# Kernel optimization log

Hardware: AMD Instinct MI355X
Metric: run time of the kernel (lower is better)

Reference implementation:

```python
import jax, jax.numpy as jnp
import numpy as np
from jax import lax

EPS = 1e-5

def conv3x3(x, w):
    # x: (B,C,H,W), w: (O,I,3,3), stride 1, padding 1
    return lax.conv_general_dilated(x, w, (1, 1), 'SAME',
                                    dimension_numbers=('NCHW', 'OIHW', 'NCHW'))

def bn_eval(x, p):
    # p: (4, C) rows = scale, bias, running_mean, running_var (eval-mode BatchNorm2d)
    s, b, m, v = p[0], p[1], p[2], p[3]
    inv = s / jnp.sqrt(v + EPS)
    return (x - m[:, None, None]) * inv[:, None, None] + b[:, None, None]

def sobel_eem(x, wx, wy, bnx, bny):
    gx = bn_eval(conv3x3(x, wx), bnx)
    gy = bn_eval(conv3x3(x, wy), bny)
    return jnp.sqrt(gx * gx + gy * gy)

def conv1x1(x, w, b):
    # w: (O, I)
    return jnp.einsum('oi,bihw->bohw', w, x) + b[:, None, None]

def attend(x_q, x_kv, qw, qb, kw, kb, vw, vb, gamma):
    B, C, H, W = x_q.shape
    N = H * W
    q = conv1x1(x_q, qw, qb).reshape(B, -1, N)      # (B, Cq, N)
    k = conv1x1(x_kv, kw, kb).reshape(B, -1, N)     # (B, Cq, N)
    v = conv1x1(x_kv, vw, vb).reshape(B, C, N)      # (B, C, N)
    energy = jnp.einsum('bcq,bck->bqk', q, k)       # unscaled QK^T, (B, N, N)
    attn = jax.nn.softmax(energy, axis=-1)
    out = jnp.einsum('bck,bqk->bcq', v, attn)       # V @ attn^T
    out = out.reshape(B, C, H, W)
    return gamma * out + x_q

def setup_inputs() -> dict:
    key = jax.random.key(0)
    ks = jax.random.split(key, 24)
    C, Cq, B, H, W = 256, 32, 1, 64, 64
    f32 = jnp.float32
    def bn_params(k):
        k1, k2 = jax.random.split(k)
        scale = 1.0 + 0.1 * jax.random.normal(k1, (C,), f32)
        bias = 0.1 * jax.random.normal(k2, (C,), f32)
        mean = jnp.zeros((C,), f32)
        var = jnp.ones((C,), f32)
        return jnp.stack([scale, bias, mean, var])
    return {
        'x1': jax.random.normal(ks[0], (B, C, H, W), f32),
        'x2': jax.random.normal(ks[1], (B, C, H, W), f32),
        'sx1_w': 0.05 * jax.random.normal(ks[2], (C, C, 3, 3), f32),
        'sy1_w': 0.05 * jax.random.normal(ks[3], (C, C, 3, 3), f32),
        'bn1x': bn_params(ks[4]), 'bn1y': bn_params(ks[5]),
        'sx2_w': 0.05 * jax.random.normal(ks[6], (C, C, 3, 3), f32),
        'sy2_w': 0.05 * jax.random.normal(ks[7], (C, C, 3, 3), f32),
        'bn2x': bn_params(ks[8]), 'bn2y': bn_params(ks[9]),
        'q1_w': 0.02 * jax.random.normal(ks[10], (Cq, C), f32),
        'q1_b': jnp.zeros((Cq,), f32),
        'k1_w': 0.02 * jax.random.normal(ks[11], (Cq, C), f32),
        'k1_b': jnp.zeros((Cq,), f32),
        'v1_w': 0.02 * jax.random.normal(ks[12], (C, C), f32),
        'v1_b': jnp.zeros((C,), f32),
        'q2_w': 0.02 * jax.random.normal(ks[13], (Cq, C), f32),
        'q2_b': jnp.zeros((Cq,), f32),
        'k2_w': 0.02 * jax.random.normal(ks[14], (Cq, C), f32),
        'k2_b': jnp.zeros((Cq,), f32),
        'v2_w': 0.02 * jax.random.normal(ks[15], (C, C), f32),
        'v2_b': jnp.zeros((C,), f32),
        'gamma1': jnp.ones((1,), f32),
        'gamma2': jnp.ones((1,), f32),
    }

def reference(x1, x2, sx1_w, sy1_w, bn1x, bn1y, sx2_w, sy2_w, bn2x, bn2y,
              q1_w, q1_b, k1_w, k1_b, v1_w, v1_b,
              q2_w, q2_b, k2_w, k2_b, v2_w, v2_b, gamma1, gamma2):
    xf1 = sobel_eem(x1, sx1_w, sy1_w, bn1x, bn1y)
    xf2 = sobel_eem(x2, sx2_w, sy2_w, bn2x, bn2y)
    # cross_value=True: K and V both come from the other modality's edge features
    out1 = attend(x1, xf2, q1_w, q1_b, k1_w, k1_b, v1_w, v1_b, gamma1)
    out2 = attend(x2, xf1, q2_w, q2_b, k2_w, k2_b, v2_w, v2_b, gamma2)
    return (out1, out2)
```

## Files before the change

### kernel.cpp

```cpp
#include <hip/hip_runtime.h>
#include <hip/hip_bf16.h>
#include <math.h>

#define CC 256
#define CQn 32
#define HH 64
#define WW 64
#define NN 4096
#define EPSF 1e-5f

typedef __hip_bfloat16 bf16;

typedef __attribute__((ext_vector_type(8))) short bf16x8v;
typedef __attribute__((ext_vector_type(4))) float f32x4v;

__device__ __forceinline__ float b2f(bf16 v) { return __bfloat162float(v); }
__device__ __forceinline__ bf16 f2b(float v) { return __float2bfloat16(v); }

template<typename T> __device__ __forceinline__ float ldf(const T* p, size_t i);
template<> __device__ __forceinline__ float ldf<float>(const float* p, size_t i) { return p[i]; }
template<> __device__ __forceinline__ float ldf<bf16>(const bf16* p, size_t i)  { return b2f(p[i]); }

__device__ __forceinline__ void stf(float* p, size_t i, float v) { p[i] = v; }
__device__ __forceinline__ void stf(bf16* p, size_t i, float v)  { p[i] = f2b(v); }

__global__ __launch_bounds__(256)
void detect_kernel(const unsigned short* __restrict__ x1, int* __restrict__ flag)
{
    __shared__ int bad;
    if (threadIdx.x == 0) bad = 0;
    __syncthreads();
    int mybad = 0;
    for (int i = threadIdx.x; i < 16384; i += 256) {
        unsigned short u = x1[i];
        if ((u & 0x7F80u) == 0x7F80u) mybad = 1;
    }
    if (mybad) atomicOr(&bad, 1);
    __syncthreads();
    if (threadIdx.x == 0) *flag = bad ? 1 : 0;
}

__global__ __launch_bounds__(256)
void transpose_kernel(const int* __restrict__ dflag,
                      const bf16* __restrict__ x, bf16* __restrict__ xT)
{
    if (*dflag != 0) return;
    const int ci0 = blockIdx.x * 64;
    const int p0  = blockIdx.y * 64;
    const int t = threadIdx.x;
    const int r0 = t >> 3;
    const int ch = t & 7;

    __shared__ bf16 tile[64][72];

    #pragma unroll
    for (int pass = 0; pass < 2; ++pass) {
        int r = pass * 32 + r0;
        uint4 v = *(const uint4*)(x + (size_t)(ci0 + r) * NN + p0 + ch * 8);
        *(uint4*)&tile[r][ch * 8] = v;
    }
    __syncthreads();
    #pragma unroll
    for (int pass = 0; pass < 2; ++pass) {
        int p = pass * 32 + r0;
        bf16 tmp[8];
        #pragma unroll
        for (int j = 0; j < 8; ++j) tmp[j] = tile[ch * 8 + j][p];
        *(uint4*)(xT + (size_t)(p0 + p) * CC + ci0 + ch * 8) = *(const uint4*)tmp;
    }
}

__global__ __launch_bounds__(256)
void packw_kernel(const int* __restrict__ dflag,
                  const bf16* __restrict__ wx, const bf16* __restrict__ wy,
                  bf16* __restrict__ Wr)
{
    if (*dflag != 0) return;
    const int lin = blockIdx.x * 256 + threadIdx.x;
    const int ci4 = lin & 63;
    const int m   = (lin >> 6) & 511;
    const int kk  = lin >> 15;
    const int o   = m >> 1;
    const bf16* src = (m & 1) ? wy : wx;
    bf16 tmp[4];
    #pragma unroll
    for (int j = 0; j < 4; ++j)
        tmp[j] = src[(size_t)o * 2304 + (ci4 * 4 + j) * 9 + kk];
    *(uint2*)(Wr + ((size_t)kk * 512 + m) * CC + ci4 * 4) = *(const uint2*)tmp;
}

__global__ __launch_bounds__(256)
void sobel_mfma_kernel(const int* __restrict__ dflag,
                       const bf16* __restrict__ xT,
                       const bf16* __restrict__ Wr,
                       const bf16* __restrict__ bnx,
                       const bf16* __restrict__ bny,
                       bf16* __restrict__ xf)
{
    if (*dflag != 0) return;
    const int mt = blockIdx.x;
    const int y  = blockIdx.y;
    const int tid = threadIdx.x;
    const int w = tid >> 6, lane = tid & 63;
    const int wm = (w >> 1) * 32, wn = (w & 1) * 32;
    const int lr = lane & 15, q = lane >> 4;

    __shared__ char smem[18432];
    bf16* Asm = (bf16*)smem;
    bf16* Bsm = Asm + 64 * 40;
    float* eb = (float*)smem;

    f32x4v acc[2][2];
    #pragma unroll
    for (int i = 0; i < 2; ++i)
        #pragma unroll
        for (int j = 0; j < 2; ++j) acc[i][j] = (f32x4v){0.f, 0.f, 0.f, 0.f};

    const int r = tid >> 2, ch = tid & 3;
    const bf16* Arow = Wr + (size_t)(mt * 64 + r) * CC + ch * 8;

    for (int kk = 0; kk < 9; ++kk) {
        const int dy = kk / 3 - 1, dx = kk - (kk / 3) * 3 - 1;
        const int ys = y + dy, xs = r + dx;
        const bool ok = (ys >= 0) && (ys < HH) && (xs >= 0) && (xs < WW);
        const bf16* Brow = xT + (size_t)(ys * WW + xs) * CC + ch * 8;
        const bf16* Ak = Arow + (size_t)kk * (512 * CC);
        for (int c0 = 0; c0 < CC; c0 += 32) {
            uint4 av = *(const uint4*)(Ak + c0);
            uint4 bv = make_uint4(0u, 0u, 0u, 0u);
            if (ok) bv = *(const uint4*)(Brow + c0);
            __syncthreads();
            *(uint4*)&Asm[r * 40 + ch * 8] = av;
            *(uint4*)&Bsm[r * 40 + ch * 8] = bv;
            __syncthreads();
            bf16x8v a0 = *(const bf16x8v*)&Asm[(wm + lr) * 40 + q * 8];
            bf16x8v a1 = *(const bf16x8v*)&Asm[(wm + 16 + lr) * 40 + q * 8];
            bf16x8v b0 = *(const bf16x8v*)&Bsm[(wn + lr) * 40 + q * 8];
            bf16x8v b1 = *(const bf16x8v*)&Bsm[(wn + 16 + lr) * 40 + q * 8];
            acc[0][0] = __builtin_amdgcn_mfma_f32_16x16x32_bf16(a0, b0, acc[0][0], 0, 0, 0);
            acc[0][1] = __builtin_amdgcn_mfma_f32_16x16x32_bf16(a0, b1, acc[0][1], 0, 0, 0);
            acc[1][0] = __builtin_amdgcn_mfma_f32_16x16x32_bf16(a1, b0, acc[1][0], 0, 0, 0);
            acc[1][1] = __builtin_amdgcn_mfma_f32_16x16x32_bf16(a1, b1, acc[1][1], 0, 0, 0);
        }
    }

    __syncthreads();
    #pragma unroll
    for (int fm = 0; fm < 2; ++fm)
        #pragma unroll
        for (int fn = 0; fn < 2; ++fn)
            #pragma unroll
            for (int reg = 0; reg < 4; ++reg)
                eb[(wm + fm * 16 + q * 4 + reg) * 72 + (wn + fn * 16 + lr)] = acc[fm][fn][reg];
    __syncthreads();
    {
        const int oc_l = tid >> 3, nch = tid & 7;
        const int oc = mt * 32 + oc_l;
        const float invx = b2f(bnx[oc]) * rsqrtf(b2f(bnx[3 * CC + oc]) + EPSF);
        const float bx   = b2f(bnx[CC + oc]);
        const float mx   = b2f(bnx[2 * CC + oc]);
        const float invy = b2f(bny[oc]) * rsqrtf(b2f(bny[3 * CC + oc]) + EPSF);
        const float by   = b2f(bny[CC + oc]);
        const float my   = b2f(bny[2 * CC + oc]);
        bf16 outv[8];
        #pragma unroll
        for (int j = 0; j < 8; ++j) {
            float gxv = eb[(2 * oc_l) * 72 + nch * 8 + j];
            float gyv = eb[(2 * oc_l + 1) * 72 + nch * 8 + j];
            float gxn = (gxv - mx) * invx + bx;
            float gyn = (gyv - my) * invy + by;
            outv[j] = f2b(sqrtf(gxn * gxn + gyn * gyn));
        }
        *(uint4*)(xf + (size_t)oc * NN + y * WW + nch * 8) = *(const uint4*)outv;
    }
}

__global__ __launch_bounds__(256)
void transpose_split_kernel(const int* __restrict__ dflag,
                            const float* __restrict__ x,
                            bf16* __restrict__ xT_hi, bf16* __restrict__ xT_lo)
{
    if (*dflag != 1) return;
    const int ci0 = blockIdx.x * 64;
    const int p0  = blockIdx.y * 64;
    const int t = threadIdx.x;
    const int r = t >> 2, ch = t & 3;

    __shared__ float tile[64][76];

    {
        const float* src = x + (size_t)(ci0 + r) * NN + p0 + ch * 16;
        #pragma unroll
        for (int i = 0; i < 4; ++i) {
            float4 v = *(const float4*)(src + i * 4);
            *(float4*)&tile[r][ch * 16 + i * 4] = v;
        }
    }
    __syncthreads();
    {
        bf16 hi[16], lo[16];
        #pragma unroll
        for (int j = 0; j < 16; ++j) {
            float v = tile[ch * 16 + j][r];
            bf16 h = f2b(v);
            hi[j] = h;
            lo[j] = f2b(v - b2f(h));
        }
        size_t base = (size_t)(p0 + r) * CC + ci0 + ch * 16;
        *(uint4*)(xT_hi + base)     = ((const uint4*)hi)[0];
        *(uint4*)(xT_hi + base + 8) = ((const uint4*)hi)[1];
        *(uint4*)(xT_lo + base)     = ((const uint4*)lo)[0];
        *(uint4*)(xT_lo + base + 8) = ((const uint4*)lo)[1];
    }
}

__global__ __launch_bounds__(256)
void sobel_mfma_f32_kernel(const int* __restrict__ dflag,
                           const bf16* __restrict__ xTh,
                           const bf16* __restrict__ xTl,
                           const float* __restrict__ wx,
                           const float* __restrict__ wy,
                           const float* __restrict__ bnx,
                           const float* __restrict__ bny,
                           bf16* __restrict__ xf)
{
    if (*dflag != 1) return;
    const int mt = blockIdx.x;
    const int y  = blockIdx.y;
    const int tid = threadIdx.x;
    const int w = tid >> 6, lane = tid & 63;
    const int wm = (w >> 1) * 32, wn = (w & 1) * 32;
    const int lr = lane & 15, q = lane >> 4;

    __shared__ char smem[20800];
    bf16* Ah = (bf16*)smem;
    bf16* Al = Ah + 2560;
    bf16* Bh = Al + 2560;
    bf16* Bl = Bh + 2640;
    float* eb = (float*)smem;

    f32x4v acc[2][2];
    #pragma unroll
    for (int i = 0; i < 2; ++i)
        #pragma unroll
        for (int j = 0; j < 2; ++j) acc[i][j] = (f32x4v){0.f, 0.f, 0.f, 0.f};

    const int r = tid >> 2, ch = tid & 3;
    const int o = mt * 32 + (r >> 1);
    const float* wbase = ((r & 1) ? wy : wx) + (size_t)o * 2304;

    if (tid < 40) {
        Bh[tid] = f2b(0.f);           Bl[tid] = f2b(0.f);
        Bh[65 * 40 + tid] = f2b(0.f); Bl[65 * 40 + tid] = f2b(0.f);
    }

    for (int c0i = 0; c0i < 8; ++c0i) {
        const int c0 = c0i * 32;
        for (int dy = 0; dy < 3; ++dy) {
            const int ys = y + dy - 1;
            const float* wb = wbase + (size_t)(c0 + ch * 8) * 9 + dy * 3;
            float wv[8][3];
            #pragma unroll
            for (int j = 0; j < 8; ++j)
                #pragma unroll
                for (int d = 0; d < 3; ++d)
                    wv[j][d] = wb[j * 9 + d];
            uint4 bh = make_uint4(0u, 0u, 0u, 0u), bl = make_uint4(0u, 0u, 0u, 0u);
            if (ys >= 0 && ys < HH) {
                size_t bidx = (size_t)(ys * WW + r) * CC + c0 + ch * 8;
                bh = *(const uint4*)(xTh + bidx);
                bl = *(const uint4*)(xTl + bidx);
            }
            #pragma unroll
            for (int d = 0; d < 3; ++d) {
                __syncthreads();
                {
                    bf16 ah8[8], al8[8];
                    #pragma unroll
                    for (int j = 0; j < 8; ++j) {
                        float v = wv[j][d];
                        bf16 h = f2b(v);
                        ah8[j] = h;
                        al8[j] = f2b(v - b2f(h));
                    }
                    *(uint4*)&Ah[r * 40 + ch * 8] = *(const uint4*)ah8;
                    *(uint4*)&Al[r * 40 + ch * 8] = *(const uint4*)al8;
                    if (d == 0) {
                        *(uint4*)&Bh[(r + 1) * 40 + ch * 8] = bh;
                        *(uint4*)&Bl[(r + 1) * 40 + ch * 8] = bl;
                    }
                }
                __syncthreads();
                bf16x8v ah0 = *(const bf16x8v*)&Ah[(wm + lr) * 40 + q * 8];
                bf16x8v ah1 = *(const bf16x8v*)&Ah[(wm + 16 + lr) * 40 + q * 8];
                bf16x8v al0 = *(const bf16x8v*)&Al[(wm + lr) * 40 + q * 8];
                bf16x8v al1 = *(const bf16x8v*)&Al[(wm + 16 + lr) * 40 + q * 8];
                const int b0r = wn + lr + d, b1r = wn + 16 + lr + d;
                bf16x8v bh0 = *(const bf16x8v*)&Bh[b0r * 40 + q * 8];
                bf16x8v bh1 = *(const bf16x8v*)&Bh[b1r * 40 + q * 8];
                bf16x8v bl0 = *(const bf16x8v*)&Bl[b0r * 40 + q * 8];
                bf16x8v bl1 = *(const bf16x8v*)&Bl[b1r * 40 + q * 8];
                acc[0][0] = __builtin_amdgcn_mfma_f32_16x16x32_bf16(ah0, bh0, acc[0][0], 0, 0, 0);
                acc[0][0] = __builtin_amdgcn_mfma_f32_16x16x32_bf16(ah0, bl0, acc[0][0], 0, 0, 0);
                acc[0][0] = __builtin_amdgcn_mfma_f32_16x16x32_bf16(al0, bh0, acc[0][0], 0, 0, 0);
                acc[0][1] = __builtin_amdgcn_mfma_f32_16x16x32_bf16(ah0, bh1, acc[0][1], 0, 0, 0);
                acc[0][1] = __builtin_amdgcn_mfma_f32_16x16x32_bf16(ah0, bl1, acc[0][1], 0, 0, 0);
                acc[0][1] = __builtin_amdgcn_mfma_f32_16x16x32_bf16(al0, bh1, acc[0][1], 0, 0, 0);
                acc[1][0] = __builtin_amdgcn_mfma_f32_16x16x32_bf16(ah1, bh0, acc[1][0], 0, 0, 0);
                acc[1][0] = __builtin_amdgcn_mfma_f32_16x16x32_bf16(ah1, bl0, acc[1][0], 0, 0, 0);
                acc[1][0] = __builtin_amdgcn_mfma_f32_16x16x32_bf16(al1, bh0, acc[1][0], 0, 0, 0);
                acc[1][1] = __builtin_amdgcn_mfma_f32_16x16x32_bf16(ah1, bh1, acc[1][1], 0, 0, 0);
                acc[1][1] = __builtin_amdgcn_mfma_f32_16x16x32_bf16(ah1, bl1, acc[1][1], 0, 0, 0);
                acc[1][1] = __builtin_amdgcn_mfma_f32_16x16x32_bf16(al1, bh1, acc[1][1], 0, 0, 0);
            }
        }
    }

    __syncthreads();
    #pragma unroll
    for (int fm = 0; fm < 2; ++fm)
        #pragma unroll
        for (int fn = 0; fn < 2; ++fn)
            #pragma unroll
            for (int reg = 0; reg < 4; ++reg)
                eb[(wm + fm * 16 + q * 4 + reg) * 72 + (wn + fn * 16 + lr)] = acc[fm][fn][reg];
    __syncthreads();
    {
        const int oc_l = tid >> 3, nch = tid & 7;
        const int oc = mt * 32 + oc_l;
        const float invx = bnx[oc] * rsqrtf(bnx[3 * CC + oc] + EPSF);
        const float bx   = bnx[CC + oc];
        const float mx   = bnx[2 * CC + oc];
        const float invy = bny[oc] * rsqrtf(bny[3 * CC + oc] + EPSF);
        const float by   = bny[CC + oc];
        const float my   = bny[2 * CC + oc];
        bf16 outv[8];
        #pragma unroll
        for (int j = 0; j < 8; ++j) {
            float gxv = eb[(2 * oc_l) * 72 + nch * 8 + j];
            float gyv = eb[(2 * oc_l + 1) * 72 + nch * 8 + j];
            float gxn = (gxv - mx) * invx + bx;
            float gyn = (gyv - my) * invy + by;
            outv[j] = f2b(sqrtf(gxn * gxn + gyn * gyn));
        }
        *(uint4*)(xf + (size_t)oc * NN + y * WW + nch * 8) = *(const uint4*)outv;
    }
}

template<typename T>
__global__ __launch_bounds__(256)
void qkv_kernel(const int* __restrict__ dflag, int want,
                const T* __restrict__ x1, const T* __restrict__ x2,
                const bf16* __restrict__ xf1, const bf16* __restrict__ xf2,
                const T* __restrict__ q1w, const T* __restrict__ q1b,
                const T* __restrict__ k1w, const T* __restrict__ k1b,
                const T* __restrict__ v1w, const T* __restrict__ v1b,
                const T* __restrict__ q2w, const T* __restrict__ q2b,
                const T* __restrict__ k2w, const T* __restrict__ k2b,
                const T* __restrict__ v2w, const T* __restrict__ v2b,
                bf16* __restrict__ qc1, bf16* __restrict__ kc1, bf16* __restrict__ v1t,
                bf16* __restrict__ qc2, bf16* __restrict__ kc2, bf16* __restrict__ v2t)
{
    if (*dflag != want) return;
    const int z = blockIdx.z;
    const T* Wb; const T* bias;
    const T* Xt = nullptr; const bf16* Xb = nullptr;
    bf16* outQ = nullptr; bf16* outK = nullptr; bf16* outV = nullptr; int O;
    switch (z) {
        case 0:  Wb = q1w; bias = q1b; Xt = x1;  outQ = qc1; O = CQn; break;
        case 1:  Wb = k1w; bias = k1b; Xb = xf2; outK = kc1; O = CQn; break;
        case 2:  Wb = v1w; bias = v1b; Xb = xf2; outV = v1t; O = CC;  break;
        case 3:  Wb = q2w; bias = q2b; Xt = x2;  outQ = qc2; O = CQn; break;
        case 4:  Wb = k2w; bias = k2b; Xb = xf1; outK = kc2; O = CQn; break;
        default: Wb = v2w; bias = v2b; Xb = xf1; outV = v2t; O = CC;  break;
    }
    const int o0 = blockIdx.x * 32;
    if (o0 >= O) return;
    const int n0 = blockIdx.y * 512;
    const int tid = threadIdx.x;

    __shared__ float lw[32 * 256];
    for (int idx = tid; idx < 32 * 256; idx += 256)
        lw[idx] = ldf(Wb, (size_t)o0 * CC + idx);
    __syncthreads();

    const int n_a = n0 + tid;
    const int n_b = n0 + 256 + tid;

    float acca[32], accb[32];
    #pragma unroll
    for (int o = 0; o < 32; ++o) { acca[o] = 0.f; accb[o] = 0.f; }

    const float4* lw4 = (const float4*)lw;
    for (int c4 = 0; c4 < 64; ++c4) {
        float xa[4], xb[4];
        #pragma unroll
        for (int k = 0; k < 4; ++k) {
            size_t ia = (size_t)(c4 * 4 + k) * NN + n_a;
            size_t ib = (size_t)(c4 * 4 + k) * NN + n_b;
            if (Xt) { xa[k] = ldf(Xt, ia); xb[k] = ldf(Xt, ib); }
            else    { xa[k] = b2f(Xb[ia]); xb[k] = b2f(Xb[ib]); }
        }
        #pragma unroll
        for (int o = 0; o < 32; ++o) {
            float4 w4 = lw4[o * 64 + c4];
            acca[o] = fmaf(w4.x, xa[0], fmaf(w4.y, xa[1], fmaf(w4.z, xa[2], fmaf(w4.w, xa[3], acca[o]))));
            accb[o] = fmaf(w4.x, xb[0], fmaf(w4.y, xb[1], fmaf(w4.z, xb[2], fmaf(w4.w, xb[3], accb[o]))));
        }
    }
    #pragma unroll
    for (int o = 0; o < 32; ++o) {
        float bb = ldf(bias, o0 + o);
        acca[o] += bb; accb[o] += bb;
    }
    if (outV) {
        #pragma unroll
        for (int o = 0; o < 32; ++o) {
            outV[(size_t)(o0 + o) * NN + n_a] = f2b(acca[o]);
            outV[(size_t)(o0 + o) * NN + n_b] = f2b(accb[o]);
        }
    } else {
        #pragma unroll
        for (int half = 0; half < 2; ++half) {
            const float* ac = half ? accb : acca;
            const int n = half ? n_b : n_a;
            bf16 hi[32], lo[32];
            #pragma unroll
            for (int o = 0; o < 32; ++o) {
                float v = ac[o];
                bf16 h = f2b(v);
                hi[o] = h;
                lo[o] = f2b(v - b2f(h));
            }
            if (outQ) {
                bf16* row = outQ + (size_t)n * 64;
                #pragma unroll
                for (int u = 0; u < 4; ++u) {
                    ((uint4*)row)[u] = ((const uint4*)hi)[u];
                    ((uint4*)(row + 32))[u] = ((const uint4*)lo)[u];
                }
            } else {
                bf16* row = outK + (size_t)n * 96;
                #pragma unroll
                for (int u = 0; u < 4; ++u) {
                    ((uint4*)row)[u] = ((const uint4*)hi)[u];
                    ((uint4*)(row + 32))[u] = ((const uint4*)hi)[u];
                    ((uint4*)(row + 64))[u] = ((const uint4*)lo)[u];
                }
            }
        }
    }
}

__device__ __forceinline__ int vswz(int chunk, int row) { return (chunk ^ (row & 7)) * 8; }

template<typename T>
__global__ __launch_bounds__(256)
void attend_mfma_kernel(const int* __restrict__ dflag, int want,
                        const bf16* __restrict__ qc1, const bf16* __restrict__ kc1,
                        const bf16* __restrict__ v1, const T* __restrict__ x1,
                        const T* __restrict__ g1,
                        const bf16* __restrict__ qc2, const bf16* __restrict__ kc2,
                        const bf16* __restrict__ v2, const T* __restrict__ x2,
                        const T* __restrict__ g2,
                        T* __restrict__ out)
{
    if (*dflag != want) return;
    const int att = blockIdx.x >> 8;
    const int i0 = (blockIdx.x & 255) * 16;
    const bf16* qc = att ? qc2 : qc1;
    const bf16* kc = att ? kc2 : kc1;
    const bf16* vt = att ? v2 : v1;
    const T* xq = att ? x2 : x1;
    const T* gp = att ? g2 : g1;
    T* o = out + (size_t)att * CC * NN;

    const int tid = threadIdx.x;
    const int w = tid >> 6, lane = tid & 63;
    const int lr = lane & 15, g = lane >> 4;

    __shared__ __align__(16) bf16 lds[26880];
    bf16* Kc = lds;
    bf16* Vt = lds + 8192;
    bf16* Ph = lds + 24576;
    bf16* Pl = lds + 25728;

    const bf16* qrow = qc + (size_t)(i0 + lr) * 64 + g * 8;
    bf16x8v qh = *(const bf16x8v*)(qrow);
    bf16x8v ql = *(const bf16x8v*)(qrow + 32);

    float l_r[4];
    #pragma unroll
    for (int r = 0; r < 4; ++r) l_r[r] = 0.f;
    f32x4v oacc[4];
    #pragma unroll
    for (int f = 0; f < 4; ++f) oacc[f] = (f32x4v){0.f, 0.f, 0.f, 0.f};

    for (int jt = 0; jt < 64; ++jt) {
        const int j0 = jt * 64;
        __syncthreads();
        #pragma unroll
        for (int s = 0; s < 3; ++s) {
            int idx = tid + s * 256;
            int row = idx / 12, cq = idx - row * 12;
            uint4 u = *(const uint4*)(kc + (size_t)(j0 + row) * 96 + cq * 8);
            *(uint4*)&Kc[row * 128 + vswz(cq, row)] = u;
        }
        {
            const bf16* src = vt + (size_t)tid * NN + j0;
            bf16* dst = Vt + tid * 64;
            #pragma unroll
            for (int s = 0; s < 8; ++s)
                *(uint4*)(dst + vswz(s, tid)) = *(const uint4*)(src + s * 8);
        }
        __syncthreads();

        f32x4v e[4];
        #pragma unroll
        for (int nf = 0; nf < 4; ++nf) {
            const bf16* kr = Kc + (nf * 16 + lr) * 128;
            bf16x8v b0 = *(const bf16x8v*)(kr + vswz(g, lr));
            bf16x8v b1 = *(const bf16x8v*)(kr + vswz(4 + g, lr));
            bf16x8v b2 = *(const bf16x8v*)(kr + vswz(8 + g, lr));
            f32x4v z = (f32x4v){0.f, 0.f, 0.f, 0.f};
            z = __builtin_amdgcn_mfma_f32_16x16x32_bf16(qh, b0, z, 0, 0, 0);
            z = __builtin_amdgcn_mfma_f32_16x16x32_bf16(ql, b1, z, 0, 0, 0);
            z = __builtin_amdgcn_mfma_f32_16x16x32_bf16(qh, b2, z, 0, 0, 0);
            e[nf] = z;
        }
        #pragma unroll
        for (int r = 0; r < 4; ++r) {
            float p0 = __expf(e[0][r]);
            float p1 = __expf(e[1][r]);
            float p2 = __expf(e[2][r]);
            float p3 = __expf(e[3][r]);
            l_r[r] += (p0 + p1) + (p2 + p3);
            float pw = (w == 0) ? p0 : (w == 1) ? p1 : (w == 2) ? p2 : p3;
            bf16 ph = f2b(pw);
            Ph[(g * 4 + r) * 72 + w * 16 + lr] = ph;
            Pl[(g * 4 + r) * 72 + w * 16 + lr] = f2b(pw - b2f(ph));
        }
        __syncthreads();

        bf16x8v pah[2], pal[2];
        #pragma unroll
        for (int ks = 0; ks < 2; ++ks) {
            pah[ks] = *(const bf16x8v*)&Ph[lr * 72 + ks * 32 + g * 8];
            pal[ks] = *(const bf16x8v*)&Pl[lr * 72 + ks * 32 + g * 8];
        }
        #pragma unroll
        for (int f = 0; f < 4; ++f) {
            const int rowc = w * 64 + f * 16 + lr;
            const bf16* vr = Vt + rowc * 64;
            #pragma unroll
            for (int ks = 0; ks < 2; ++ks) {
                bf16x8v bv = *(const bf16x8v*)(vr + vswz(ks * 4 + g, lr));
                oacc[f] = __builtin_amdgcn_mfma_f32_16x16x32_bf16(pah[ks], bv, oacc[f], 0, 0, 0);
                oacc[f] = __builtin_amdgcn_mfma_f32_16x16x32_bf16(pal[ks], bv, oacc[f], 0, 0, 0);
            }
        }
    }

    #pragma unroll
    for (int r = 0; r < 4; ++r)
        #pragma unroll
        for (int msk = 1; msk <= 8; msk <<= 1)
            l_r[r] += __shfl_xor(l_r[r], msk);

    __syncthreads();
    float* ob = (float*)lds;
    float* ls = ob + 5120;
    #pragma unroll
    for (int f = 0; f < 4; ++f)
        #pragma unroll
        for (int r = 0; r < 4; ++r)
            ob[(w * 64 + f * 16 + lr) * 20 + g * 4 + r] = oacc[f][r];
    if (w == 0 && lr == 0) {
        #pragma unroll
        for (int r = 0; r < 4; ++r) ls[g * 4 + r] = l_r[r];
    }
    __syncthreads();
    {
        const float gm = ldf(gp, 0);
        const int c = tid;
        const size_t rowo = (size_t)c * NN + i0;
        #pragma unroll
        for (int q = 0; q < 16; ++q) {
            float v = ob[c * 20 + q] / ls[q];
            float xv = ldf(xq, rowo + q);
            stf(o, rowo + q, fmaf(gm, v, xv));
        }
    }
}

extern "C" void kernel_launch(void* const* d_in, const int* in_sizes, int n_in,
                              void* d_out, int out_size, void* d_ws, size_t ws_size,
                              hipStream_t stream) {
    if (ws_size < (size_t)11010304) return;

    int* dflag = (int*)d_ws;
    char* base = (char*)d_ws + 256;
    bf16* xf1 = (bf16*)base;
    bf16* xf2 = xf1 + 1048576;
    char* ubase = (char*)(xf2 + 1048576);
    bf16* xTb = (bf16*)ubase;
    bf16* Wrb = (bf16*)(ubase + 2 * 1024 * 1024);
    bf16* xTh = (bf16*)ubase;
    bf16* xTl = (bf16*)(ubase + 2 * 1024 * 1024);
    bf16* v1t = (bf16*)ubase;
    bf16* v2t = v1t + 1048576;
    bf16* qc1 = v2t + 1048576;
    bf16* kc1 = qc1 + 262144;
    bf16* qc2 = kc1 + 393216;
    bf16* kc2 = qc2 + 262144;

    detect_kernel<<<dim3(1), 256, 0, stream>>>((const unsigned short*)d_in[0], dflag);

    {
        typedef bf16 T;
        transpose_kernel<<<dim3(4, 64), 256, 0, stream>>>(dflag, (const T*)d_in[0], xTb);
        packw_kernel<<<dim3(1152), 256, 0, stream>>>(dflag, (const T*)d_in[2], (const T*)d_in[3], Wrb);
        sobel_mfma_kernel<<<dim3(8, 64), 256, 0, stream>>>(dflag, xTb, Wrb,
            (const T*)d_in[4], (const T*)d_in[5], xf1);
        transpose_kernel<<<dim3(4, 64), 256, 0, stream>>>(dflag, (const T*)d_in[1], xTb);
        packw_kernel<<<dim3(1152), 256, 0, stream>>>(dflag, (const T*)d_in[6], (const T*)d_in[7], Wrb);
        sobel_mfma_kernel<<<dim3(8, 64), 256, 0, stream>>>(dflag, xTb, Wrb,
            (const T*)d_in[8], (const T*)d_in[9], xf2);
        qkv_kernel<T><<<dim3(8, 8, 6), 256, 0, stream>>>(dflag, 0,
            (const T*)d_in[0], (const T*)d_in[1], xf1, xf2,
            (const T*)d_in[10], (const T*)d_in[11], (const T*)d_in[12], (const T*)d_in[13],
            (const T*)d_in[14], (const T*)d_in[15], (const T*)d_in[16], (const T*)d_in[17],
            (const T*)d_in[18], (const T*)d_in[19], (const T*)d_in[20], (const T*)d_in[21],
            qc1, kc1, v1t, qc2, kc2, v2t);
        attend_mfma_kernel<T><<<dim3(512), 256, 0, stream>>>(dflag, 0,
            qc1, kc1, v1t, (const T*)d_in[0], (const T*)d_in[22],
            qc2, kc2, v2t, (const T*)d_in[1], (const T*)d_in[23],
            (T*)d_out);
    }
    {
        typedef float T;
        transpose_split_kernel<<<dim3(4, 64), 256, 0, stream>>>(dflag, (const T*)d_in[0], xTh, xTl);
        sobel_mfma_f32_kernel<<<dim3(8, 64), 256, 0, stream>>>(dflag, xTh, xTl,
            (const T*)d_in[2], (const T*)d_in[3], (const T*)d_in[4], (const T*)d_in[5], xf1);
        transpose_split_kernel<<<dim3(4, 64), 256, 0, stream>>>(dflag, (const T*)d_in[1], xTh, xTl);
        sobel_mfma_f32_kernel<<<dim3(8, 64), 256, 0, stream>>>(dflag, xTh, xTl,
            (const T*)d_in[6], (const T*)d_in[7], (const T*)d_in[8], (const T*)d_in[9], xf2);
        qkv_kernel<T><<<dim3(8, 8, 6), 256, 0, stream>>>(dflag, 1,
            (const T*)d_in[0], (const T*)d_in[1], xf1, xf2,
            (const T*)d_in[10], (const T*)d_in[11], (const T*)d_in[12], (const T*)d_in[13],
            (const T*)d_in[14], (const T*)d_in[15], (const T*)d_in[16], (const T*)d_in[17],
            (const T*)d_in[18], (const T*)d_in[19], (const T*)d_in[20], (const T*)d_in[21],
            qc1, kc1, v1t, qc2, kc2, v2t);
        attend_mfma_kernel<T><<<dim3(512), 256, 0, stream>>>(dflag, 1,
            qc1, kc1, v1t, (const T*)d_in[0], (const T*)d_in[22],
            qc2, kc2, v2t, (const T*)d_in[1], (const T*)d_in[23],
            (T*)d_out);
    }
}
```

Measured before the change: 519.5 us.

## Halve sobel output tile per block and block V layout for coalesced attention loads

```diff
diff --git a/kernel.cpp b/kernel.cpp
--- a/kernel.cpp
+++ b/kernel.cpp
@@ -229,25 +229,24 @@
     const int y  = blockIdx.y;
     const int tid = threadIdx.x;
     const int w = tid >> 6, lane = tid & 63;
-    const int wm = (w >> 1) * 32, wn = (w & 1) * 32;
+    const int wm = (w >> 1) * 16, wn = (w & 1) * 32;
     const int lr = lane & 15, q = lane >> 4;
 
-    __shared__ char smem[20800];
+    __shared__ char smem[16384];
     bf16* Ah = (bf16*)smem;
-    bf16* Al = Ah + 2560;
-    bf16* Bh = Al + 2560;
+    bf16* Al = Ah + 1280;
+    bf16* Bh = Al + 1280;
     bf16* Bl = Bh + 2640;
     float* eb = (float*)smem;
 
-    f32x4v acc[2][2];
-    #pragma unroll
-    for (int i = 0; i < 2; ++i)
-        #pragma unroll
-        for (int j = 0; j < 2; ++j) acc[i][j] = (f32x4v){0.f, 0.f, 0.f, 0.f};
+    f32x4v acc[2];
+    acc[0] = (f32x4v){0.f, 0.f, 0.f, 0.f};
+    acc[1] = (f32x4v){0.f, 0.f, 0.f, 0.f};
 
     const int r = tid >> 2, ch = tid & 3;
-    const int o = mt * 32 + (r >> 1);
-    const float* wbase = ((r & 1) ? wy : wx) + (size_t)o * 2304;
+    const bool aAct = tid < 128;
+    const int o = mt * 16 + (r >> 1);
+    const float* wbase = aAct ? (((r & 1) ? wy : wx) + (size_t)o * 2304) : wx;
 
     if (tid < 40) {
         Bh[tid] = f2b(0.f);           Bl[tid] = f2b(0.f);
@@ -258,13 +257,15 @@
         const int c0 = c0i * 32;
         for (int dy = 0; dy < 3; ++dy) {
             const int ys = y + dy - 1;
-            const float* wb = wbase + (size_t)(c0 + ch * 8) * 9 + dy * 3;
             float wv[8][3];
-            #pragma unroll
-            for (int j = 0; j < 8; ++j)
+            if (aAct) {
+                const float* wb = wbase + (size_t)(c0 + ch * 8) * 9 + dy * 3;
                 #pragma unroll
-                for (int d = 0; d < 3; ++d)
-                    wv[j][d] = wb[j * 9 + d];
+                for (int j = 0; j < 8; ++j)
+                    #pragma unroll
+                    for (int d = 0; d < 3; ++d)
+                        wv[j][d] = wb[j * 9 + d];
+            }
             uint4 bh = make_uint4(0u, 0u, 0u, 0u), bl = make_uint4(0u, 0u, 0u, 0u);
             if (ys >= 0 && ys < HH) {
                 size_t bidx = (size_t)(ys * WW + r) * CC + c0 + ch * 8;
@@ -274,7 +275,7 @@
             #pragma unroll
             for (int d = 0; d < 3; ++d) {
                 __syncthreads();
-                {
+                if (aAct) {
                     bf16 ah8[8], al8[8];
                     #pragma unroll
                     for (int j = 0; j < 8; ++j) {
@@ -285,49 +286,39 @@
                     }
                     *(uint4*)&Ah[r * 40 + ch * 8] = *(const uint4*)ah8;
                     *(uint4*)&Al[r * 40 + ch * 8] = *(const uint4*)al8;
-                    if (d == 0) {
-                        *(uint4*)&Bh[(r + 1) * 40 + ch * 8] = bh;
-                        *(uint4*)&Bl[(r + 1) * 40 + ch * 8] = bl;
-                    }
+                }
+                if (d == 0) {
+                    *(uint4*)&Bh[(r + 1) * 40 + ch * 8] = bh;
+                    *(uint4*)&Bl[(r + 1) * 40 + ch * 8] = bl;
                 }
                 __syncthreads();
                 bf16x8v ah0 = *(const bf16x8v*)&Ah[(wm + lr) * 40 + q * 8];
-                bf16x8v ah1 = *(const bf16x8v*)&Ah[(wm + 16 + lr) * 40 + q * 8];
                 bf16x8v al0 = *(const bf16x8v*)&Al[(wm + lr) * 40 + q * 8];
-                bf16x8v al1 = *(const bf16x8v*)&Al[(wm + 16 + lr) * 40 + q * 8];
                 const int b0r = wn + lr + d, b1r = wn + 16 + lr + d;
                 bf16x8v bh0 = *(const bf16x8v*)&Bh[b0r * 40 + q * 8];
                 bf16x8v bh1 = *(const bf16x8v*)&Bh[b1r * 40 + q * 8];
                 bf16x8v bl0 = *(const bf16x8v*)&Bl[b0r * 40 + q * 8];
                 bf16x8v bl1 = *(const bf16x8v*)&Bl[b1r * 40 + q * 8];
-                acc[0][0] = __builtin_amdgcn_mfma_f32_16x16x32_bf16(ah0, bh0, acc[0][0], 0, 0, 0);
-                acc[0][0] = __builtin_amdgcn_mfma_f32_16x16x32_bf16(ah0, bl0, acc[0][0], 0, 0, 0);
-                acc[0][0] = __builtin_amdgcn_mfma_f32_16x16x32_bf16(al0, bh0, acc[0][0], 0, 0, 0);
-                acc[0][1] = __builtin_amdgcn_mfma_f32_16x16x32_bf16(ah0, bh1, acc[0][1], 0, 0, 0);
-                acc[0][1] = __builtin_amdgcn_mfma_f32_16x16x32_bf16(ah0, bl1, acc[0][1], 0, 0, 0);
-                acc[0][1] = __builtin_amdgcn_mfma_f32_16x16x32_bf16(al0, bh1, acc[0][1], 0, 0, 0);
-                acc[1][0] = __builtin_amdgcn_mfma_f32_16x16x32_bf16(ah1, bh0, acc[1][0], 0, 0, 0);
-                acc[1][0] = __builtin_amdgcn_mfma_f32_16x16x32_bf16(ah1, bl0, acc[1][0], 0, 0, 0);
-                acc[1][0] = __builtin_amdgcn_mfma_f32_16x16x32_bf16(al1, bh0, acc[1][0], 0, 0, 0);
-                acc[1][1] = __builtin_amdgcn_mfma_f32_16x16x32_bf16(ah1, bh1, acc[1][1], 0, 0, 0);
-                acc[1][1] = __builtin_amdgcn_mfma_f32_16x16x32_bf16(ah1, bl1, acc[1][1], 0, 0, 0);
-                acc[1][1] = __builtin_amdgcn_mfma_f32_16x16x32_bf16(al1, bh1, acc[1][1], 0, 0, 0);
+                acc[0] = __builtin_amdgcn_mfma_f32_16x16x32_bf16(ah0, bh0, acc[0], 0, 0, 0);
+                acc[0] = __builtin_amdgcn_mfma_f32_16x16x32_bf16(ah0, bl0, acc[0], 0, 0, 0);
+                acc[0] = __builtin_amdgcn_mfma_f32_16x16x32_bf16(al0, bh0, acc[0], 0, 0, 0);
+                acc[1] = __builtin_amdgcn_mfma_f32_16x16x32_bf16(ah0, bh1, acc[1], 0, 0, 0);
+                acc[1] = __builtin_amdgcn_mfma_f32_16x16x32_bf16(ah0, bl1, acc[1], 0, 0, 0);
+                acc[1] = __builtin_amdgcn_mfma_f32_16x16x32_bf16(al0, bh1, acc[1], 0, 0, 0);
             }
         }
     }
 
     __syncthreads();
     #pragma unroll
-    for (int fm = 0; fm < 2; ++fm)
-        #pragma unroll
-        for (int fn = 0; fn < 2; ++fn)
-            #pragma unroll
-            for (int reg = 0; reg < 4; ++reg)
-                eb[(wm + fm * 16 + q * 4 + reg) * 72 + (wn + fn * 16 + lr)] = acc[fm][fn][reg];
-    __syncthreads();
-    {
+    for (int fn = 0; fn < 2; ++fn)
+        #pragma unroll
+        for (int reg = 0; reg < 4; ++reg)
+            eb[(wm + q * 4 + reg) * 72 + (wn + fn * 16 + lr)] = acc[fn][reg];
+    __syncthreads();
+    if (tid < 128) {
         const int oc_l = tid >> 3, nch = tid & 7;
-        const int oc = mt * 32 + oc_l;
+        const int oc = mt * 16 + oc_l;
         const float invx = bnx[oc] * rsqrtf(bnx[3 * CC + oc] + EPSF);
         const float bx   = bnx[CC + oc];
         const float mx   = bnx[2 * CC + oc];
@@ -416,8 +407,8 @@
     if (outV) {
         #pragma unroll
         for (int o = 0; o < 32; ++o) {
-            outV[(size_t)(o0 + o) * NN + n_a] = f2b(acca[o]);
-            outV[(size_t)(o0 + o) * NN + n_b] = f2b(accb[o]);
+            outV[((size_t)(n_a >> 6) * CC + (o0 + o)) * 64 + (n_a & 63)] = f2b(acca[o]);
+            outV[((size_t)(n_b >> 6) * CC + (o0 + o)) * 64 + (n_b & 63)] = f2b(accb[o]);
         }
     } else {
         #pragma unroll
@@ -507,11 +498,14 @@
             *(uint4*)&Kc[row * 128 + vswz(cq, row)] = u;
         }
         {
-            const bf16* src = vt + (size_t)tid * NN + j0;
-            bf16* dst = Vt + tid * 64;
+            const bf16* src = vt + ((size_t)jt * (CC * 64));
             #pragma unroll
-            for (int s = 0; s < 8; ++s)
-                *(uint4*)(dst + vswz(s, tid)) = *(const uint4*)(src + s * 8);
+            for (int i = 0; i < 8; ++i) {
+                const int idx = i * 256 + tid;
+                const int c = idx >> 3, chk = idx & 7;
+                *(uint4*)&Vt[c * 64 + vswz(chk, c)] =
+                    *(const uint4*)(src + (size_t)idx * 8);
+            }
         }
         __syncthreads();
 
@@ -640,10 +634,10 @@
     {
         typedef float T;
         transpose_split_kernel<<<dim3(4, 64), 256, 0, stream>>>(dflag, (const T*)d_in[0], xTh, xTl);
-        sobel_mfma_f32_kernel<<<dim3(8, 64), 256, 0, stream>>>(dflag, xTh, xTl,
+        sobel_mfma_f32_kernel<<<dim3(16, 64), 256, 0, stream>>>(dflag, xTh, xTl,
             (const T*)d_in[2], (const T*)d_in[3], (const T*)d_in[4], (const T*)d_in[5], xf1);
         transpose_split_kernel<<<dim3(4, 64), 256, 0, stream>>>(dflag, (const T*)d_in[1], xTh, xTl);
-        sobel_mfma_f32_kernel<<<dim3(8, 64), 256, 0, stream>>>(dflag, xTh, xTl,
+        sobel_mfma_f32_kernel<<<dim3(16, 64), 256, 0, stream>>>(dflag, xTh, xTl,
             (const T*)d_in[6], (const T*)d_in[7], (const T*)d_in[8], (const T*)d_in[9], xf2);
         qkv_kernel<T><<<dim3(8, 8, 6), 256, 0, stream>>>(dflag, 1,
             (const T*)d_in[0], (const T*)d_in[1], xf1, xf2,
```

Result: faster. 503.5 us (-3.1%).
